# Kernel tuning notes

Measured on AMD Instinct MI355X. Metric: run time of the kernel, lower is better.

Reference implementation:

```python
import jax, jax.numpy as jnp
import numpy as np

L = 50            # self.length
ARG = 5           # argument_limit
OUT = 3 * L + 5   # output_size = 155
VOC = 100         # max_embeddings
B = 4096          # batch of formulas
LEAVES = 64       # predicate leaves per tree (depth-6 binary tree)
LEVEL_OFFSETS = [0, 32, 48, 56, 60, 62]  # op_ids offsets, bottom-up levels


def setup_inputs() -> dict:
    key = jax.random.key(0)
    ks = jax.random.split(key, 12)
    s = 0.05
    return {
        "pred_ids": jax.random.randint(ks[0], (B, LEAVES), 0, VOC),
        "arg_ids": jax.random.randint(ks[1], (B, LEAVES, ARG), 0, VOC),
        "op_ids": jax.random.randint(ks[2], (B, LEAVES - 1), 0, VOC),
        "emb_pred": jax.random.normal(ks[3], (VOC, L), jnp.float32),
        "emb_var": jax.random.normal(ks[4], (VOC, L), jnp.float32),
        "emb_op": jax.random.normal(ks[5], (VOC, L), jnp.float32),
        "W_pred": jax.random.normal(ks[6], (L, (1 + ARG) * L), jnp.float32) * s,
        "b_pred": jnp.zeros((L,), jnp.float32),
        "W_bin": jax.random.normal(ks[7], (L, 3 * L), jnp.float32) * s,
        "b_bin": jnp.zeros((L,), jnp.float32),
        "W_final": jax.random.normal(ks[8], (OUT, L), jnp.float32) * s,
        "b_final": jnp.zeros((OUT,), jnp.float32),
    }


def reference(pred_ids, arg_ids, op_ids, emb_pred, emb_var, emb_op,
              W_pred, b_pred, W_bin, b_bin, W_final, b_final):
    # Leaf terms: plain embedding lookup (visit_encoded_element)
    args = emb_var[arg_ids]                         # [B, LEAVES, ARG, L]
    pred = emb_pred[pred_ids]                       # [B, LEAVES, L]
    cat = jnp.concatenate([pred, args.reshape(B, LEAVES, ARG * L)], axis=-1)
    # visit_predicate_expression: relu(Linear(concat))
    x = jax.nn.relu(cat @ W_pred.T + b_pred)        # [B, LEAVES, L]
    # Bottom-up binary-formula levels: relu(Linear(concat(left, op, right)))
    for off in LEVEL_OFFSETS:
        n = x.shape[1] // 2
        left, right = x[:, 0::2], x[:, 1::2]        # [B, n, L]
        op = emb_op[op_ids[:, off:off + n]]         # [B, n, L]
        x = jax.nn.relu(
            jnp.concatenate([left, op, right], axis=-1) @ W_bin.T + b_bin)
    # forward: self.final(self.visit(input)) at tree root
    return x[:, 0] @ W_final.T + b_final            # [B, OUT]
```

## Files before the change

kernel.cpp:

```cpp
#include <hip/hip_runtime.h>

using short8 = __attribute__((ext_vector_type(8))) short;
using h8     = __attribute__((ext_vector_type(8))) _Float16;
using h2     = __attribute__((ext_vector_type(2))) _Float16;
using f32x4  = __attribute__((ext_vector_type(4))) float;

#define NB  16
#define NTH 512
#define WBIN_OFF 0
#define WFIN_OFF 12288
#define EMBO_OFF 22528
#define LTAB_OFF 28928
#define WS_USHORTS 67328

__device__ __forceinline__ unsigned short f2h_bits(float v) {
    _Float16 h = (_Float16)v;
    return *reinterpret_cast<unsigned short*>(&h);
}
__device__ __forceinline__ h8 ld8h(const unsigned short* p) {
    return *reinterpret_cast<const h8*>(p);
}
__device__ __forceinline__ short8 ld8s(const unsigned short* p) {
    return *reinterpret_cast<const short8*>(p);
}
__device__ __forceinline__ f32x4 mf(h8 a, h8 b, f32x4 c) {
    return __builtin_amdgcn_mfma_f32_16x16x32_f16(a, b, c, 0, 0, 0);
}

__global__ void prep_kernel(const float* __restrict__ emb_pred,
                            const float* __restrict__ emb_var,
                            const float* __restrict__ emb_op,
                            const float* __restrict__ W_pred,
                            const float* __restrict__ W_bin,
                            const float* __restrict__ W_final,
                            unsigned short* __restrict__ ws) {
    for (int i = blockIdx.x * blockDim.x + threadIdx.x; i < WS_USHORTS;
         i += gridDim.x * blockDim.x) {
        float v = 0.f;
        if (i < WFIN_OFF) {
            int n = i / 192, k = i - n * 192, p = k >> 6, j = k & 63;
            if (n < 50 && j < 50) v = W_bin[n * 150 + p * 50 + j];
        } else if (i < EMBO_OFF) {
            int t = i - WFIN_OFF, o = t >> 6, k = t & 63;
            if (o < 155 && k < 50) v = W_final[o * 50 + k];
        } else if (i < LTAB_OFF) {
            int t = i - EMBO_OFF, r = t >> 6, j = t & 63;
            if (j < 50) v = emb_op[r * 50 + j];
        } else {
            int t = i - LTAB_OFF;
            int p = t / 6400, rest = t - p * 6400, vv = rest >> 6, n = rest & 63;
            if (n < 50) {
                const float* e = (p == 0) ? (emb_pred + vv * 50) : (emb_var + vv * 50);
                const float* wr = W_pred + n * 300 + p * 50;
                float acc = 0.f;
                for (int k = 0; k < 50; ++k) acc += e[k] * wr[k];
                v = acc;
            }
        }
        ws[i] = f2h_bits(v);
    }
}

#define TNODE(NT0, NTN, CL, CR, GN, DST) do {                                   \
    const unsigned short* rl_ = s_x[CL];                                        \
    const unsigned short* rr_ = s_x[CR];                                        \
    int r_ = s_op[(GN) * 16 + l15];                                             \
    h8 aL0 = ld8h(rl_ + l15 * 64 + ((quad ^ (l15 & 7)) << 3));                  \
    h8 aL1 = ld8h(rl_ + l15 * 64 + (((quad + 4) ^ (l15 & 7)) << 3));            \
    h8 aO0 = ld8h(s_embop + r_ * 64 + ((quad ^ (r_ & 7)) << 3));                \
    h8 aO1 = ld8h(s_embop + r_ * 64 + (((quad + 4) ^ (r_ & 7)) << 3));          \
    h8 aR0 = ld8h(rr_ + l15 * 64 + ((quad ^ (l15 & 7)) << 3));                  \
    h8 aR1 = ld8h(rr_ + l15 * 64 + (((quad + 4) ^ (l15 & 7)) << 3));            \
    f32x4 acc_[NTN];                                                            \
    _Pragma("unroll") for (int i_ = 0; i_ < (NTN); ++i_) {                      \
        acc_[i_] = (f32x4){0.f, 0.f, 0.f, 0.f};                                 \
        acc_[i_] = mf(aL0, wb[0][0][(NT0) + i_], acc_[i_]);                     \
        acc_[i_] = mf(aL1, wb[0][1][(NT0) + i_], acc_[i_]);                     \
        acc_[i_] = mf(aO0, wb[1][0][(NT0) + i_], acc_[i_]);                     \
        acc_[i_] = mf(aO1, wb[1][1][(NT0) + i_], acc_[i_]);                     \
        acc_[i_] = mf(aR0, wb[2][0][(NT0) + i_], acc_[i_]);                     \
        acc_[i_] = mf(aR1, wb[2][1][(NT0) + i_], acc_[i_]);                     \
    }                                                                           \
    unsigned short* drow_ = s_x[DST];                                           \
    _Pragma("unroll") for (int i_ = 0; i_ < (NTN); ++i_) {                      \
        int n_ = ((NT0) + i_) * 16 + l15;                                       \
        _Pragma("unroll") for (int q_ = 0; q_ < 4; ++q_) {                      \
            int m_ = quad * 4 + q_;                                             \
            float v_ = fmaxf(acc_[i_][q_] + biasb[(NT0) + i_], 0.f);            \
            drow_[m_ * 64 + (((n_ >> 3) ^ (m_ & 7)) << 3) + (n_ & 7)] = f2h_bits(v_); \
        }                                                                       \
    }                                                                           \
} while (0)

__global__ __launch_bounds__(NTH, 2) void formula_kernel(
    const int* __restrict__ pred_ids, const int* __restrict__ arg_ids,
    const int* __restrict__ op_ids,
    const float* __restrict__ b_pred, const float* __restrict__ b_bin,
    const float* __restrict__ b_final,
    const unsigned short* __restrict__ ws,
    float* __restrict__ out)
{
    __shared__ __align__(16) unsigned short s_ltab[6 * 100 * 64];
    __shared__ __align__(16) unsigned short s_embop[100 * 64];
    __shared__ __align__(16) unsigned short s_x[31][1024];
    __shared__ __align__(8)  unsigned char  s_ids[64][16][8];
    __shared__ unsigned char s_op[64 * 16];

    const int tid  = threadIdx.x;
    const int b0   = blockIdx.x * NB;
    const int lane = tid & 63;
    const int w    = tid >> 6;
    const int l15  = lane & 15;
    const int quad = lane >> 4;
    const int cg   = tid & 7;

    for (int i = tid; i < 6 * 100 * 8; i += NTH)
        *reinterpret_cast<short8*>(&s_ltab[i * 8]) = ld8s(ws + LTAB_OFF + i * 8);
    for (int i = tid; i < 100 * 8; i += NTH) {
        int r = i >> 3, s = i & 7;
        *reinterpret_cast<short8*>(&s_embop[r * 64 + ((s ^ (r & 7)) << 3)]) =
            ld8s(ws + EMBO_OFF + r * 64 + s * 8);
    }
    for (int e = tid; e < 64 * 16; e += NTH) {
        int lf = e >> 4, m = e & 15;
        unsigned char* rec = &s_ids[lf][m][0];
        rec[0] = (unsigned char)pred_ids[(b0 + m) * 64 + lf];
        #pragma unroll
        for (int a = 0; a < 5; ++a)
            rec[1 + a] = (unsigned char)arg_ids[(b0 + m) * 320 + lf * 5 + a];
        rec[6] = 0; rec[7] = 0;
    }
    for (int e = tid; e < 63 * 16; e += NTH) {
        int r = e >> 4, m = e & 15;
        s_op[r * 16 + m] = (unsigned char)op_ids[(b0 + m) * 63 + r];
    }

    short8 wb_raw[3][2][4];
    #pragma unroll
    for (int p = 0; p < 3; ++p)
        #pragma unroll
        for (int h = 0; h < 2; ++h)
            #pragma unroll
            for (int nt = 0; nt < 4; ++nt)
                wb_raw[p][h][nt] = ld8s(ws + WBIN_OFF + (nt * 16 + l15) * 192
                                        + p * 64 + (quad + 4 * h) * 8);
    h8 (&wb)[3][2][4] = reinterpret_cast<h8(&)[3][2][4]>(wb_raw);

    float biasb[4];
    #pragma unroll
    for (int nt = 0; nt < 4; ++nt) {
        int n = nt * 16 + l15;
        biasb[nt] = (n < 50) ? b_bin[n] : 0.f;
    }
    h2 bias2[4];
    #pragma unroll
    for (int k = 0; k < 4; ++k) {
        int n0 = cg * 8 + 2 * k, n1 = n0 + 1;
        bias2[k] = (h2){(_Float16)((n0 < 50) ? b_pred[n0] : 0.f),
                        (_Float16)((n1 < 50) ? b_pred[n1] : 0.f)};
    }
    const h2 z2 = (h2){(_Float16)0.f, (_Float16)0.f};

    __syncthreads();

    for (int st = 0; st < 4; ++st) {
        #pragma unroll
        for (int p4 = 0; p4 < 4; ++p4) {
            int job = p4 * NTH + tid;
            int lfl = job >> 7;
            int m   = (job >> 3) & 15;
            int lf  = st * 16 + lfl;
            const unsigned int* ivp =
                reinterpret_cast<const unsigned int*>(&s_ids[lf][m][0]);
            unsigned int ix = ivp[0], iy = ivp[1];
            int r0 = ix & 255, r1 = (ix >> 8) & 255, r2 = (ix >> 16) & 255;
            int r3 = ix >> 24, r4 = iy & 255, r5 = (iy >> 8) & 255;
            h2 a0 = bias2[0], a1 = bias2[1], a2 = bias2[2], a3 = bias2[3];
            #define ACCT(ROW, P) {                                              \
                h8 t_ = ld8h(s_ltab + (P) * 6400 + (ROW) * 64 + cg * 8);        \
                const h2* tp_ = reinterpret_cast<const h2*>(&t_);               \
                a0 += tp_[0]; a1 += tp_[1]; a2 += tp_[2]; a3 += tp_[3]; }
            ACCT(r0, 0); ACCT(r1, 1); ACCT(r2, 2);
            ACCT(r3, 3); ACCT(r4, 4); ACCT(r5, 5);
            #undef ACCT
            a0 = __builtin_elementwise_max(a0, z2);
            a1 = __builtin_elementwise_max(a1, z2);
            a2 = __builtin_elementwise_max(a2, z2);
            a3 = __builtin_elementwise_max(a3, z2);
            union { h2 h[4]; short8 s; } u;
            u.h[0] = a0; u.h[1] = a1; u.h[2] = a2; u.h[3] = a3;
            *reinterpret_cast<short8*>(
                &s_x[lfl][m * 64 + ((cg ^ (m & 7)) << 3)]) = u.s;
        }
        __syncthreads();
        TNODE(0, 4, 2 * w, 2 * w + 1, st * 8 + w, 16 + w);
        __syncthreads();
        {
            int j = w >> 1;
            int cl = 16 + 2 * j, cr = 17 + 2 * j, gn = 32 + st * 4 + j, dst = j;
            if ((w & 1) == 0) TNODE(0, 2, cl, cr, gn, dst);
            else              TNODE(2, 2, cl, cr, gn, dst);
        }
        __syncthreads();
        {
            int j = w >> 2;
            int cl = 2 * j, cr = 2 * j + 1, gn = 48 + st * 2 + j, dst = 16 + j;
            switch (w & 3) {
                case 0: TNODE(0, 1, cl, cr, gn, dst); break;
                case 1: TNODE(1, 1, cl, cr, gn, dst); break;
                case 2: TNODE(2, 1, cl, cr, gn, dst); break;
                default: TNODE(3, 1, cl, cr, gn, dst); break;
            }
        }
        __syncthreads();
        if (w < 4) {
            int gn = 56 + st, dst = 24 + st;
            switch (w) {
                case 0: TNODE(0, 1, 16, 17, gn, dst); break;
                case 1: TNODE(1, 1, 16, 17, gn, dst); break;
                case 2: TNODE(2, 1, 16, 17, gn, dst); break;
                default: TNODE(3, 1, 16, 17, gn, dst); break;
            }
        }
        __syncthreads();
    }
    {
        int gg = w >> 2;
        int cl = 24 + 2 * gg, cr = 25 + 2 * gg, gn = 60 + gg, dst = 28 + gg;
        switch (w & 3) {
            case 0: TNODE(0, 1, cl, cr, gn, dst); break;
            case 1: TNODE(1, 1, cl, cr, gn, dst); break;
            case 2: TNODE(2, 1, cl, cr, gn, dst); break;
            default: TNODE(3, 1, cl, cr, gn, dst); break;
        }
    }
    __syncthreads();
    if (w < 4) {
        switch (w) {
            case 0: TNODE(0, 1, 28, 29, 62, 30); break;
            case 1: TNODE(1, 1, 28, 29, 62, 30); break;
            case 2: TNODE(2, 1, 28, 29, 62, 30); break;
            default: TNODE(3, 1, 28, 29, 62, 30); break;
        }
    }
    __syncthreads();

    auto headtile = [&](int t) {
        f32x4 acc = {0.f, 0.f, 0.f, 0.f};
        int n2 = t * 16 + l15;
        const unsigned short* rroot = s_x[30];
        h8 x0 = ld8h(rroot + l15 * 64 + ((quad ^ (l15 & 7)) << 3));
        h8 x1 = ld8h(rroot + l15 * 64 + (((quad + 4) ^ (l15 & 7)) << 3));
        acc = mf(x0, ld8h(ws + WFIN_OFF + n2 * 64 + quad * 8), acc);
        acc = mf(x1, ld8h(ws + WFIN_OFF + n2 * 64 + (quad + 4) * 8), acc);
        if (n2 < 155) {
            float bias = b_final[n2];
            #pragma unroll
            for (int q = 0; q < 4; ++q) {
                int m = quad * 4 + q;
                out[(b0 + m) * 155 + n2] = acc[q] + bias;
            }
        }
    };
    headtile(w);
    if (w < 2) headtile(8 + w);
}

extern "C" void kernel_launch(void* const* d_in, const int* in_sizes, int n_in,
                              void* d_out, int out_size, void* d_ws, size_t ws_size,
                              hipStream_t stream) {
    const int*   pred_ids = (const int*)  d_in[0];
    const int*   arg_ids  = (const int*)  d_in[1];
    const int*   op_ids   = (const int*)  d_in[2];
    const float* emb_pred = (const float*)d_in[3];
    const float* emb_var  = (const float*)d_in[4];
    const float* emb_op   = (const float*)d_in[5];
    const float* W_pred   = (const float*)d_in[6];
    const float* b_pred   = (const float*)d_in[7];
    const float* W_bin    = (const float*)d_in[8];
    const float* b_bin    = (const float*)d_in[9];
    const float* W_final  = (const float*)d_in[10];
    const float* b_final  = (const float*)d_in[11];
    unsigned short* ws = (unsigned short*)d_ws;
    float* out = (float*)d_out;

    hipLaunchKernelGGL(prep_kernel, dim3(256), dim3(256), 0, stream,
                       emb_pred, emb_var, emb_op, W_pred, W_bin, W_final, ws);
    hipLaunchKernelGGL(formula_kernel, dim3(4096 / NB), dim3(NTH), 0, stream,
                       pred_ids, arg_ids, op_ids, b_pred, b_bin, b_final,
                       (const unsigned short*)ws, out);
}
```

Measured before the change: 35.60 us.

## Process all leaves in one pass with 1024 threads, read leaf table from global

The block size doubles to 1024 threads, and the four-stage subtree loop becomes a single pass. All 64 leaves are computed at once into a 64-slot activation buffer, and the tree is then reduced level by level in place, so far fewer barriers are needed. The per-leaf projection table is no longer staged in LDS; leaf accumulation reads it directly from the workspace in global memory, which frees LDS for the larger activation buffer. The cost is more global/L2 gather traffic for the leaf stage. The stricter launch bound may also force tighter register limits and cause spills of the preloaded weight fragments.

```diff
diff --git a/kernel.cpp b/kernel.cpp
--- a/kernel.cpp
+++ b/kernel.cpp
@@ -6,7 +6,7 @@
 using f32x4  = __attribute__((ext_vector_type(4))) float;
 
 #define NB  16
-#define NTH 512
+#define NTH 1024
 #define WBIN_OFF 0
 #define WFIN_OFF 12288
 #define EMBO_OFF 22528
@@ -92,7 +92,7 @@
     }                                                                           \
 } while (0)
 
-__global__ __launch_bounds__(NTH, 2) void formula_kernel(
+__global__ __launch_bounds__(NTH, 4) void formula_kernel(
     const int* __restrict__ pred_ids, const int* __restrict__ arg_ids,
     const int* __restrict__ op_ids,
     const float* __restrict__ b_pred, const float* __restrict__ b_bin,
@@ -100,11 +100,10 @@
     const unsigned short* __restrict__ ws,
     float* __restrict__ out)
 {
-    __shared__ __align__(16) unsigned short s_ltab[6 * 100 * 64];
+    __shared__ __align__(16) unsigned short s_x[64][1024];
     __shared__ __align__(16) unsigned short s_embop[100 * 64];
-    __shared__ __align__(16) unsigned short s_x[31][1024];
     __shared__ __align__(8)  unsigned char  s_ids[64][16][8];
-    __shared__ unsigned char s_op[64 * 16];
+    __shared__ unsigned char s_op[63 * 16 + 16];
 
     const int tid  = threadIdx.x;
     const int b0   = blockIdx.x * NB;
@@ -114,15 +113,13 @@
     const int quad = lane >> 4;
     const int cg   = tid & 7;
 
-    for (int i = tid; i < 6 * 100 * 8; i += NTH)
-        *reinterpret_cast<short8*>(&s_ltab[i * 8]) = ld8s(ws + LTAB_OFF + i * 8);
-    for (int i = tid; i < 100 * 8; i += NTH) {
-        int r = i >> 3, s = i & 7;
+    if (tid < 800) {
+        int r = tid >> 3, s = tid & 7;
         *reinterpret_cast<short8*>(&s_embop[r * 64 + ((s ^ (r & 7)) << 3)]) =
             ld8s(ws + EMBO_OFF + r * 64 + s * 8);
     }
-    for (int e = tid; e < 64 * 16; e += NTH) {
-        int lf = e >> 4, m = e & 15;
+    {
+        int m = tid >> 6, lf = tid & 63;
         unsigned char* rec = &s_ids[lf][m][0];
         rec[0] = (unsigned char)pred_ids[(b0 + m) * 64 + lf];
         #pragma unroll
@@ -130,8 +127,8 @@
             rec[1 + a] = (unsigned char)arg_ids[(b0 + m) * 320 + lf * 5 + a];
         rec[6] = 0; rec[7] = 0;
     }
-    for (int e = tid; e < 63 * 16; e += NTH) {
-        int r = e >> 4, m = e & 15;
+    if (tid < 63 * 16) {
+        int r = tid >> 4, m = tid & 15;
         s_op[r * 16 + m] = (unsigned char)op_ids[(b0 + m) * 63 + r];
     }
 
@@ -163,92 +160,83 @@
 
     __syncthreads();
 
-    for (int st = 0; st < 4; ++st) {
-        #pragma unroll
-        for (int p4 = 0; p4 < 4; ++p4) {
-            int job = p4 * NTH + tid;
-            int lfl = job >> 7;
-            int m   = (job >> 3) & 15;
-            int lf  = st * 16 + lfl;
-            const unsigned int* ivp =
-                reinterpret_cast<const unsigned int*>(&s_ids[lf][m][0]);
-            unsigned int ix = ivp[0], iy = ivp[1];
-            int r0 = ix & 255, r1 = (ix >> 8) & 255, r2 = (ix >> 16) & 255;
-            int r3 = ix >> 24, r4 = iy & 255, r5 = (iy >> 8) & 255;
-            h2 a0 = bias2[0], a1 = bias2[1], a2 = bias2[2], a3 = bias2[3];
-            #define ACCT(ROW, P) {                                              \
-                h8 t_ = ld8h(s_ltab + (P) * 6400 + (ROW) * 64 + cg * 8);        \
-                const h2* tp_ = reinterpret_cast<const h2*>(&t_);               \
-                a0 += tp_[0]; a1 += tp_[1]; a2 += tp_[2]; a3 += tp_[3]; }
-            ACCT(r0, 0); ACCT(r1, 1); ACCT(r2, 2);
-            ACCT(r3, 3); ACCT(r4, 4); ACCT(r5, 5);
-            #undef ACCT
-            a0 = __builtin_elementwise_max(a0, z2);
-            a1 = __builtin_elementwise_max(a1, z2);
-            a2 = __builtin_elementwise_max(a2, z2);
-            a3 = __builtin_elementwise_max(a3, z2);
-            union { h2 h[4]; short8 s; } u;
-            u.h[0] = a0; u.h[1] = a1; u.h[2] = a2; u.h[3] = a3;
-            *reinterpret_cast<short8*>(
-                &s_x[lfl][m * 64 + ((cg ^ (m & 7)) << 3)]) = u.s;
-        }
-        __syncthreads();
-        TNODE(0, 4, 2 * w, 2 * w + 1, st * 8 + w, 16 + w);
-        __syncthreads();
-        {
-            int j = w >> 1;
-            int cl = 16 + 2 * j, cr = 17 + 2 * j, gn = 32 + st * 4 + j, dst = j;
-            if ((w & 1) == 0) TNODE(0, 2, cl, cr, gn, dst);
-            else              TNODE(2, 2, cl, cr, gn, dst);
-        }
-        __syncthreads();
-        {
-            int j = w >> 2;
-            int cl = 2 * j, cr = 2 * j + 1, gn = 48 + st * 2 + j, dst = 16 + j;
-            switch (w & 3) {
-                case 0: TNODE(0, 1, cl, cr, gn, dst); break;
-                case 1: TNODE(1, 1, cl, cr, gn, dst); break;
-                case 2: TNODE(2, 1, cl, cr, gn, dst); break;
-                default: TNODE(3, 1, cl, cr, gn, dst); break;
-            }
-        }
-        __syncthreads();
-        if (w < 4) {
-            int gn = 56 + st, dst = 24 + st;
-            switch (w) {
-                case 0: TNODE(0, 1, 16, 17, gn, dst); break;
-                case 1: TNODE(1, 1, 16, 17, gn, dst); break;
-                case 2: TNODE(2, 1, 16, 17, gn, dst); break;
-                default: TNODE(3, 1, 16, 17, gn, dst); break;
-            }
-        }
-        __syncthreads();
-    }
+    #pragma unroll
+    for (int p4 = 0; p4 < 8; ++p4) {
+        int jj  = p4 * 128 + (tid >> 3);
+        int lf  = jj >> 4;
+        int m   = jj & 15;
+        const unsigned int* ivp =
+            reinterpret_cast<const unsigned int*>(&s_ids[lf][m][0]);
+        unsigned int ix = ivp[0], iy = ivp[1];
+        int r0 = ix & 255, r1 = (ix >> 8) & 255, r2 = (ix >> 16) & 255;
+        int r3 = ix >> 24, r4 = iy & 255, r5 = (iy >> 8) & 255;
+        h2 a0 = bias2[0], a1 = bias2[1], a2 = bias2[2], a3 = bias2[3];
+        #define ACCT(ROW, P) {                                                  \
+            h8 t_ = ld8h(ws + LTAB_OFF + (P) * 6400 + (ROW) * 64 + cg * 8);     \
+            const h2* tp_ = reinterpret_cast<const h2*>(&t_);                   \
+            a0 += tp_[0]; a1 += tp_[1]; a2 += tp_[2]; a3 += tp_[3]; }
+        ACCT(r0, 0); ACCT(r1, 1); ACCT(r2, 2);
+        ACCT(r3, 3); ACCT(r4, 4); ACCT(r5, 5);
+        #undef ACCT
+        a0 = __builtin_elementwise_max(a0, z2);
+        a1 = __builtin_elementwise_max(a1, z2);
+        a2 = __builtin_elementwise_max(a2, z2);
+        a3 = __builtin_elementwise_max(a3, z2);
+        union { h2 h[4]; short8 s; } u;
+        u.h[0] = a0; u.h[1] = a1; u.h[2] = a2; u.h[3] = a3;
+        *reinterpret_cast<short8*>(
+            &s_x[lf][m * 64 + ((cg ^ (m & 7)) << 3)]) = u.s;
+    }
+    __syncthreads();
+
+    #pragma unroll
+    for (int i = 0; i < 2; ++i) {
+        int j = w + 16 * i;
+        TNODE(0, 4, 2 * j, 2 * j + 1, j, 2 * j);
+    }
+    __syncthreads();
+    { int j = w; TNODE(0, 4, 4 * j, 4 * j + 2, 32 + j, 4 * j); }
+    __syncthreads();
     {
-        int gg = w >> 2;
-        int cl = 24 + 2 * gg, cr = 25 + 2 * gg, gn = 60 + gg, dst = 28 + gg;
+        int j = w >> 1;
+        if ((w & 1) == 0) TNODE(0, 2, 8 * j, 8 * j + 4, 48 + j, 8 * j + 1);
+        else              TNODE(2, 2, 8 * j, 8 * j + 4, 48 + j, 8 * j + 1);
+    }
+    __syncthreads();
+    {
+        int j = w >> 2;
         switch (w & 3) {
-            case 0: TNODE(0, 1, cl, cr, gn, dst); break;
-            case 1: TNODE(1, 1, cl, cr, gn, dst); break;
-            case 2: TNODE(2, 1, cl, cr, gn, dst); break;
-            default: TNODE(3, 1, cl, cr, gn, dst); break;
+            case 0: TNODE(0, 1, 16 * j + 1, 16 * j + 9, 56 + j, 16 * j + 2); break;
+            case 1: TNODE(1, 1, 16 * j + 1, 16 * j + 9, 56 + j, 16 * j + 2); break;
+            case 2: TNODE(2, 1, 16 * j + 1, 16 * j + 9, 56 + j, 16 * j + 2); break;
+            default: TNODE(3, 1, 16 * j + 1, 16 * j + 9, 56 + j, 16 * j + 2); break;
+        }
+    }
+    __syncthreads();
+    if (w < 8) {
+        int j = w >> 2;
+        switch (w & 3) {
+            case 0: TNODE(0, 1, 32 * j + 2, 32 * j + 18, 60 + j, 32 * j + 3); break;
+            case 1: TNODE(1, 1, 32 * j + 2, 32 * j + 18, 60 + j, 32 * j + 3); break;
+            case 2: TNODE(2, 1, 32 * j + 2, 32 * j + 18, 60 + j, 32 * j + 3); break;
+            default: TNODE(3, 1, 32 * j + 2, 32 * j + 18, 60 + j, 32 * j + 3); break;
         }
     }
     __syncthreads();
     if (w < 4) {
         switch (w) {
-            case 0: TNODE(0, 1, 28, 29, 62, 30); break;
-            case 1: TNODE(1, 1, 28, 29, 62, 30); break;
-            case 2: TNODE(2, 1, 28, 29, 62, 30); break;
-            default: TNODE(3, 1, 28, 29, 62, 30); break;
-        }
-    }
-    __syncthreads();
-
-    auto headtile = [&](int t) {
+            case 0: TNODE(0, 1, 3, 35, 62, 1); break;
+            case 1: TNODE(1, 1, 3, 35, 62, 1); break;
+            case 2: TNODE(2, 1, 3, 35, 62, 1); break;
+            default: TNODE(3, 1, 3, 35, 62, 1); break;
+        }
+    }
+    __syncthreads();
+
+    if (w < 10) {
         f32x4 acc = {0.f, 0.f, 0.f, 0.f};
-        int n2 = t * 16 + l15;
-        const unsigned short* rroot = s_x[30];
+        int n2 = w * 16 + l15;
+        const unsigned short* rroot = s_x[1];
         h8 x0 = ld8h(rroot + l15 * 64 + ((quad ^ (l15 & 7)) << 3));
         h8 x1 = ld8h(rroot + l15 * 64 + (((quad + 4) ^ (l15 & 7)) << 3));
         acc = mf(x0, ld8h(ws + WFIN_OFF + n2 * 64 + quad * 8), acc);
@@ -261,9 +249,7 @@
                 out[(b0 + m) * 155 + n2] = acc[q] + bias;
             }
         }
-    };
-    headtile(w);
-    if (w < 2) headtile(8 + w);
+    }
 }
 
 extern "C" void kernel_launch(void* const* d_in, const int* in_sizes, int n_in,
```

After: 79.60 us. 2.24x slower.
